# Optimization experiments

Measured on AMD Instinct MI355X. Metric: run time of the kernel, lower is better.

## Reference

```python
import jax, jax.numpy as jnp
import numpy as np
from jax import lax

T, H, F, E, K = 4096, 1024, 2048, 8, 2

def setup_inputs() -> dict:
    key = jax.random.key(0)
    k1, k2, k3, k4 = jax.random.split(key, 4)
    return {
        "hidden_states": jax.random.normal(k1, (T, H), jnp.float32),
        "gate_w": jax.random.normal(k2, (E, H), jnp.float32) * 0.02,
        "w1": jax.random.normal(k3, (E, 2 * F, H), jnp.float32) * 0.02,  # fused gate+up
        "w2": jax.random.normal(k4, (E, H, F), jnp.float32) * 0.02,      # down proj
        "top_k": K,
    }

def reference(hidden_states, gate_w, w1, w2, top_k):
    tokens = hidden_states.shape[0]
    # Router gate (Linear, no bias)
    router_logits = hidden_states @ gate_w.T                     # [T, E]
    probs = jax.nn.softmax(router_logits.astype(jnp.float32), axis=-1)
    topk_w, topk_idx = lax.top_k(probs, top_k)                   # [T, K]
    topk_w = topk_w / jnp.sum(topk_w, axis=-1, keepdims=True)    # renormalize
    # Dense combine weights [T, E] (zero for unselected experts)
    combine = jnp.zeros_like(probs).at[jnp.arange(tokens)[:, None], topk_idx].add(topk_w)
    combine = combine.astype(hidden_states.dtype)

    def expert_step(acc, ew):
        w1_e, w2_e, c_e = ew                                     # [2F,H], [H,F], [T]
        h = hidden_states @ w1_e.T                               # [T, 2F]
        g, u = jnp.split(h, 2, axis=-1)
        y = (jax.nn.silu(g) * u) @ w2_e.T                        # [T, H]
        return acc + c_e[:, None] * y, None

    acc0 = jnp.zeros_like(hidden_states)
    final_hidden_states, _ = lax.scan(expert_step, acc0, (w1, w2, combine.T))
    return final_hidden_states, router_logits
```

## Files before the change

### kernel.cpp

```cpp
#include <hip/hip_runtime.h>

#define T 4096
#define Hdim 1024
#define Fdim 2048
#define NE 8
#define TOPK 2
#define TK (T*TOPK)

typedef unsigned short ushort_t;
typedef __attribute__((ext_vector_type(8))) short bf16x8;
typedef __attribute__((ext_vector_type(4))) float floatx4;

__device__ __forceinline__ ushort_t f2bf(float f) {
    unsigned u = __float_as_uint(f);
    u += 0x7fff + ((u >> 16) & 1);
    return (ushort_t)(u >> 16);
}
__device__ __forceinline__ uint4 cvt8(const float4 a, const float4 b) {
    uint4 r;
    r.x = (unsigned)f2bf(a.x) | ((unsigned)f2bf(a.y) << 16);
    r.y = (unsigned)f2bf(a.z) | ((unsigned)f2bf(a.w) << 16);
    r.z = (unsigned)f2bf(b.x) | ((unsigned)f2bf(b.y) << 16);
    r.w = (unsigned)f2bf(b.z) | ((unsigned)f2bf(b.w) << 16);
    return r;
}
__device__ __forceinline__ void gld16(const ushort_t* g, short* l) {
    __builtin_amdgcn_global_load_lds((const __attribute__((address_space(1))) void*)g,
                                     (__attribute__((address_space(3))) void*)l, 16, 0, 0);
}

__global__ __launch_bounds__(256) void init_kernel(float* __restrict__ out, int* __restrict__ counts) {
    long i = (long)blockIdx.x * 256 + threadIdx.x;
    float4 z = make_float4(0.f, 0.f, 0.f, 0.f);
    *(float4*)&out[i * 4] = z;
    if (blockIdx.x == 0 && threadIdx.x < NE) counts[threadIdx.x] = 0;
}

__global__ __launch_bounds__(256) void cvt_kernel(const float* __restrict__ src,
                                                  ushort_t* __restrict__ dst, long n8) {
    long stride = (long)gridDim.x * 256;
    for (long i = (long)blockIdx.x * 256 + threadIdx.x; i < n8; i += stride) {
        float4 a = *(const float4*)(src + i * 8);
        float4 b = *(const float4*)(src + i * 8 + 4);
        *(uint4*)(dst + i * 8) = cvt8(a, b);
    }
}

__global__ __launch_bounds__(64) void router_kernel(
    const float* __restrict__ hs, const float* __restrict__ gw,
    float* __restrict__ logits_out,
    int* __restrict__ counts, int* __restrict__ tok_slot, float* __restrict__ tok_wt)
{
    const int t = blockIdx.x;
    const int lane = threadIdx.x;

    float hreg[16];
#pragma unroll
    for (int i = 0; i < 16; ++i)
        hreg[i] = hs[(long)t * Hdim + lane + 64 * i];

    float acc[NE];
#pragma unroll
    for (int e = 0; e < NE; ++e) {
        float s = 0.f;
#pragma unroll
        for (int i = 0; i < 16; ++i)
            s += hreg[i] * gw[e * Hdim + lane + 64 * i];
#pragma unroll
        for (int off = 32; off > 0; off >>= 1)
            s += __shfl_xor(s, off, 64);
        acc[e] = s;
    }

    if (lane < NE) logits_out[t * NE + lane] = acc[lane];

    if (lane == 0) {
        int i1 = 0;
#pragma unroll
        for (int e = 1; e < NE; ++e) if (acc[e] > acc[i1]) i1 = e;
        int i2 = -1;
#pragma unroll
        for (int e = 0; e < NE; ++e) {
            if (e == i1) continue;
            if (i2 < 0 || acc[e] > acc[i2]) i2 = e;
        }
        float p2 = __expf(acc[i2] - acc[i1]);
        float z  = 1.f + p2;
        int pos1 = atomicAdd(&counts[i1], 1);
        tok_slot[i1 * T + pos1] = t * TOPK + 0;
        tok_wt [i1 * T + pos1] = 1.f / z;
        int pos2 = atomicAdd(&counts[i2], 1);
        tok_slot[i2 * T + pos2] = t * TOPK + 1;
        tok_wt [i2 * T + pos2] = p2 / z;
    }
}

__global__ __launch_bounds__(256) void gemm1_kernel(
    const ushort_t* __restrict__ hsb, const ushort_t* __restrict__ w1b,
    const int* __restrict__ counts, const int* __restrict__ tok_slot,
    ushort_t* __restrict__ actb)
{
    const int e = blockIdx.z;
    const int cnt = counts[e];
    const int row0 = blockIdx.y * 128;
    if (row0 >= cnt) return;
    const int f0 = blockIdx.x * 64;

    __shared__ short As[128 * 32];
    __shared__ short Bs[128 * 32];
    __shared__ int slotLds[128];

    const int tid = threadIdx.x;
    if (tid < 128) {
        int idx = row0 + tid;
        slotLds[tid] = (idx < cnt) ? tok_slot[e * T + idx] : -1;
    }
    __syncthreads();

    const int rA0 = tid >> 2,      rA1 = 64 + (tid >> 2);
    const int seg = (tid & 3) * 8;
    int s0 = slotLds[rA0], s1 = slotLds[rA1];
    const ushort_t* srcA0 = hsb + (long)((s0 >= 0 ? (s0 >> 1) : 0)) * Hdim + seg;
    const ushort_t* srcA1 = hsb + (long)((s1 >= 0 ? (s1 >> 1) : 0)) * Hdim + seg;
    const ushort_t* srcB0 = w1b + ((long)e * 2 * Fdim + (f0 + rA0)) * Hdim + seg;
    const ushort_t* srcB1 = w1b + ((long)e * 2 * Fdim + Fdim + (f0 + rA0)) * Hdim + seg;

    const int lane = tid & 63;
    const int w = tid >> 6;
    const int wm = (w >> 1) * 64;
    const int wn = (w & 1) * 32;
    const int fr = lane & 15, fg = lane >> 4;

    floatx4 accg[4][2] = {};
    floatx4 accu[4][2] = {};

    for (int k0 = 0; k0 < Hdim; k0 += 32) {
        __syncthreads();
        gld16(srcA0 + k0, &As[tid * 8]);
        gld16(srcA1 + k0, &As[(256 + tid) * 8]);
        gld16(srcB0 + k0, &Bs[tid * 8]);
        gld16(srcB1 + k0, &Bs[(256 + tid) * 8]);
        __syncthreads();

        bf16x8 a[4], g[2], u[2];
#pragma unroll
        for (int ms = 0; ms < 4; ++ms)
            a[ms] = *(bf16x8*)&As[(wm + ms * 16 + fr) * 32 + fg * 8];
#pragma unroll
        for (int ns = 0; ns < 2; ++ns) {
            g[ns] = *(bf16x8*)&Bs[(wn + ns * 16 + fr) * 32 + fg * 8];
            u[ns] = *(bf16x8*)&Bs[(64 + wn + ns * 16 + fr) * 32 + fg * 8];
        }
#pragma unroll
        for (int ms = 0; ms < 4; ++ms)
#pragma unroll
            for (int ns = 0; ns < 2; ++ns) {
                accg[ms][ns] = __builtin_amdgcn_mfma_f32_16x16x32_bf16(a[ms], g[ns], accg[ms][ns], 0, 0, 0);
                accu[ms][ns] = __builtin_amdgcn_mfma_f32_16x16x32_bf16(a[ms], u[ns], accu[ms][ns], 0, 0, 0);
            }
    }

#pragma unroll
    for (int ms = 0; ms < 4; ++ms)
#pragma unroll
        for (int ns = 0; ns < 2; ++ns)
#pragma unroll
            for (int j = 0; j < 4; ++j) {
                int m = wm + ms * 16 + fg * 4 + j;
                int slot = slotLds[m];
                if (slot >= 0) {
                    int fcol = f0 + wn + ns * 16 + fr;
                    float gv = accg[ms][ns][j];
                    float uv = accu[ms][ns][j];
                    float av = (gv / (1.f + __expf(-gv))) * uv;
                    actb[(long)slot * Fdim + fcol] = f2bf(av);
                }
            }
}

__global__ __launch_bounds__(256) void gemm2_kernel(
    const ushort_t* __restrict__ actb, const ushort_t* __restrict__ w2b,
    const int* __restrict__ counts, const int* __restrict__ tok_slot,
    const float* __restrict__ tok_wt, float* __restrict__ out)
{
    const int e = blockIdx.z;
    const int cnt = counts[e];
    const int row0 = blockIdx.y * 128;
    if (row0 >= cnt) return;
    const int h0 = blockIdx.x * 128;

    __shared__ short As[128 * 32];
    __shared__ short Bs[128 * 32];
    __shared__ int   slotLds[128];
    __shared__ float wtLds[128];

    const int tid = threadIdx.x;
    if (tid < 128) {
        int idx = row0 + tid;
        bool ok = idx < cnt;
        slotLds[tid] = ok ? tok_slot[e * T + idx] : -1;
        wtLds[tid]   = ok ? tok_wt [e * T + idx] : 0.f;
    }
    __syncthreads();

    const int rA0 = tid >> 2, rA1 = 64 + (tid >> 2);
    const int seg = (tid & 3) * 8;
    int s0 = slotLds[rA0], s1 = slotLds[rA1];
    const ushort_t* srcA0 = actb + (long)(s0 >= 0 ? s0 : 0) * Fdim + seg;
    const ushort_t* srcA1 = actb + (long)(s1 >= 0 ? s1 : 0) * Fdim + seg;
    const ushort_t* srcB0 = w2b + ((long)e * Hdim + (h0 + rA0)) * Fdim + seg;
    const ushort_t* srcB1 = w2b + ((long)e * Hdim + (h0 + rA1)) * Fdim + seg;

    const int lane = tid & 63;
    const int w = tid >> 6;
    const int wm = (w >> 1) * 64;
    const int wn = (w & 1) * 64;
    const int fr = lane & 15, fg = lane >> 4;

    floatx4 acc[4][4] = {};

    for (int k0 = 0; k0 < Fdim; k0 += 32) {
        __syncthreads();
        gld16(srcA0 + k0, &As[tid * 8]);
        gld16(srcA1 + k0, &As[(256 + tid) * 8]);
        gld16(srcB0 + k0, &Bs[tid * 8]);
        gld16(srcB1 + k0, &Bs[(256 + tid) * 8]);
        __syncthreads();

        bf16x8 a[4], b[4];
#pragma unroll
        for (int ms = 0; ms < 4; ++ms)
            a[ms] = *(bf16x8*)&As[(wm + ms * 16 + fr) * 32 + fg * 8];
#pragma unroll
        for (int ns = 0; ns < 4; ++ns)
            b[ns] = *(bf16x8*)&Bs[(wn + ns * 16 + fr) * 32 + fg * 8];
#pragma unroll
        for (int ms = 0; ms < 4; ++ms)
#pragma unroll
            for (int ns = 0; ns < 4; ++ns)
                acc[ms][ns] = __builtin_amdgcn_mfma_f32_16x16x32_bf16(a[ms], b[ns], acc[ms][ns], 0, 0, 0);
    }

#pragma unroll
    for (int ms = 0; ms < 4; ++ms)
#pragma unroll
        for (int ns = 0; ns < 4; ++ns)
#pragma unroll
            for (int j = 0; j < 4; ++j) {
                int m = wm + ms * 16 + fg * 4 + j;
                int slot = slotLds[m];
                if (slot >= 0) {
                    int t = slot >> 1;
                    int hcol = h0 + wn + ns * 16 + fr;
                    atomicAdd(&out[(long)t * Hdim + hcol], acc[ms][ns][j] * wtLds[m]);
                }
            }
}

extern "C" void kernel_launch(void* const* d_in, const int* in_sizes, int n_in,
                              void* d_out, int out_size, void* d_ws, size_t ws_size,
                              hipStream_t stream)
{
    const float* hs = (const float*)d_in[0];
    const float* gw = (const float*)d_in[1];
    const float* w1 = (const float*)d_in[2];
    const float* w2 = (const float*)d_in[3];

    float* out        = (float*)d_out;
    float* logits_out = out + (long)T * Hdim;

    char* ws = (char*)d_ws;
    size_t off = 0;
    int* counts = (int*)(ws + off);          off += 256;
    int* tok_slot = (int*)(ws + off);        off += (size_t)NE * T * sizeof(int);
    float* tok_wt = (float*)(ws + off);      off += (size_t)NE * T * sizeof(float);
    off = (off + 255) & ~(size_t)255;
    ushort_t* hsb = (ushort_t*)(ws + off);   off += (size_t)T * Hdim * sizeof(ushort_t);
    off = (off + 255) & ~(size_t)255;
    ushort_t* w1b = (ushort_t*)(ws + off);   off += (size_t)NE * 2 * Fdim * Hdim * sizeof(ushort_t);
    ushort_t* w2b = w1b;
    off = (off + 255) & ~(size_t)255;
    ushort_t* actb = (ushort_t*)(ws + off);  off += (size_t)TK * Fdim * sizeof(ushort_t);

    init_kernel<<<(int)((long)T * Hdim / 4 / 256), 256, 0, stream>>>(out, counts);
    cvt_kernel<<<1024, 256, 0, stream>>>(hs, hsb, (long)T * Hdim / 8);
    cvt_kernel<<<2048, 256, 0, stream>>>(w1, w1b, (long)NE * 2 * Fdim * Hdim / 8);
    router_kernel<<<T, 64, 0, stream>>>(hs, gw, logits_out, counts, tok_slot, tok_wt);
    gemm1_kernel<<<dim3(Fdim / 64, T / 128, NE), 256, 0, stream>>>(hsb, w1b, counts, tok_slot, actb);
    cvt_kernel<<<2048, 256, 0, stream>>>(w2, w2b, (long)NE * Hdim * Fdim / 8);
    gemm2_kernel<<<dim3(Hdim / 128, T / 128, NE), 256, 0, stream>>>(actb, w2b, counts, tok_slot, tok_wt, out);
}
```

Baseline: 531.5 us.

## Replace atomic scatter-add in down-projection with per-slot partials and combine kernel

Result: no change. 527.9 us (-0.7%).

```diff
diff --git a/kernel.cpp b/kernel.cpp
--- a/kernel.cpp
+++ b/kernel.cpp
@@ -29,11 +29,8 @@
                                      (__attribute__((address_space(3))) void*)l, 16, 0, 0);
 }
 
-__global__ __launch_bounds__(256) void init_kernel(float* __restrict__ out, int* __restrict__ counts) {
-    long i = (long)blockIdx.x * 256 + threadIdx.x;
-    float4 z = make_float4(0.f, 0.f, 0.f, 0.f);
-    *(float4*)&out[i * 4] = z;
-    if (blockIdx.x == 0 && threadIdx.x < NE) counts[threadIdx.x] = 0;
+__global__ void init_kernel(int* __restrict__ counts) {
+    if (threadIdx.x < NE) counts[threadIdx.x] = 0;
 }
 
 __global__ __launch_bounds__(256) void cvt_kernel(const float* __restrict__ src,
@@ -181,7 +178,7 @@
 __global__ __launch_bounds__(256) void gemm2_kernel(
     const ushort_t* __restrict__ actb, const ushort_t* __restrict__ w2b,
     const int* __restrict__ counts, const int* __restrict__ tok_slot,
-    const float* __restrict__ tok_wt, float* __restrict__ out)
+    const float* __restrict__ tok_wt, float* __restrict__ partial)
 {
     const int e = blockIdx.z;
     const int cnt = counts[e];
@@ -250,11 +247,23 @@
                 int m = wm + ms * 16 + fg * 4 + j;
                 int slot = slotLds[m];
                 if (slot >= 0) {
-                    int t = slot >> 1;
                     int hcol = h0 + wn + ns * 16 + fr;
-                    atomicAdd(&out[(long)t * Hdim + hcol], acc[ms][ns][j] * wtLds[m]);
+                    partial[(long)slot * Hdim + hcol] = acc[ms][ns][j] * wtLds[m];
                 }
             }
+}
+
+__global__ __launch_bounds__(256) void combine_kernel(
+    const float* __restrict__ partial, float* __restrict__ out)
+{
+    long i = (long)blockIdx.x * 256 + threadIdx.x;
+    int t  = (int)(i / (Hdim / 4));
+    int h4 = (int)(i % (Hdim / 4));
+    const float4 p0 = *(const float4*)&partial[(long)(2 * t    ) * Hdim + h4 * 4];
+    const float4 p1 = *(const float4*)&partial[(long)(2 * t + 1) * Hdim + h4 * 4];
+    float4 s;
+    s.x = p0.x + p1.x; s.y = p0.y + p1.y; s.z = p0.z + p1.z; s.w = p0.w + p1.w;
+    *(float4*)&out[(long)t * Hdim + h4 * 4] = s;
 }
 
 extern "C" void kernel_launch(void* const* d_in, const int* in_sizes, int n_in,
@@ -277,16 +286,19 @@
     off = (off + 255) & ~(size_t)255;
     ushort_t* hsb = (ushort_t*)(ws + off);   off += (size_t)T * Hdim * sizeof(ushort_t);
     off = (off + 255) & ~(size_t)255;
-    ushort_t* w1b = (ushort_t*)(ws + off);   off += (size_t)NE * 2 * Fdim * Hdim * sizeof(ushort_t);
-    ushort_t* w2b = w1b;
+    char* w1region = ws + off;               off += (size_t)NE * 2 * Fdim * Hdim * sizeof(ushort_t);
+    ushort_t* w1b = (ushort_t*)w1region;
+    ushort_t* w2b = (ushort_t*)w1region;
+    float* partial = (float*)(w1region + (size_t)NE * Hdim * Fdim * sizeof(ushort_t));
     off = (off + 255) & ~(size_t)255;
     ushort_t* actb = (ushort_t*)(ws + off);  off += (size_t)TK * Fdim * sizeof(ushort_t);
 
-    init_kernel<<<(int)((long)T * Hdim / 4 / 256), 256, 0, stream>>>(out, counts);
+    init_kernel<<<1, 64, 0, stream>>>(counts);
     cvt_kernel<<<1024, 256, 0, stream>>>(hs, hsb, (long)T * Hdim / 8);
     cvt_kernel<<<2048, 256, 0, stream>>>(w1, w1b, (long)NE * 2 * Fdim * Hdim / 8);
     router_kernel<<<T, 64, 0, stream>>>(hs, gw, logits_out, counts, tok_slot, tok_wt);
     gemm1_kernel<<<dim3(Fdim / 64, T / 128, NE), 256, 0, stream>>>(hsb, w1b, counts, tok_slot, actb);
     cvt_kernel<<<2048, 256, 0, stream>>>(w2, w2b, (long)NE * Hdim * Fdim / 8);
-    gemm2_kernel<<<dim3(Hdim / 128, T / 128, NE), 256, 0, stream>>>(actb, w2b, counts, tok_slot, tok_wt, out);
-}
+    gemm2_kernel<<<dim3(Hdim / 128, T / 128, NE), 256, 0, stream>>>(actb, w2b, counts, tok_slot, tok_wt, partial);
+    combine_kernel<<<(int)((long)T * Hdim / 4 / 256), 256, 0, stream>>>(partial, out);
+}
```
